# Kernel tuning notes

Hardware: AMD Instinct MI355X
Metric: run time of the kernel (lower is better)

The kernel has to match this reference:

```python
import jax, jax.numpy as jnp
import numpy as np

D_MODEL = 1024
DK = 64
H = D_MODEL // DK
EPS = 1e-5


def setup_inputs() -> dict:
    key = jax.random.key(0)
    ks = jax.random.split(key, 8)
    B, M = 4, 2048
    s = 1.0 / np.sqrt(D_MODEL)
    return {
        "inp": jax.random.normal(ks[0], (B, M, D_MODEL), dtype=jnp.float32),
        "Wq": jax.random.normal(ks[1], (D_MODEL, D_MODEL), dtype=jnp.float32) * s,
        "bq": jnp.zeros((D_MODEL,), dtype=jnp.float32),
        "Wk": jax.random.normal(ks[2], (D_MODEL, D_MODEL), dtype=jnp.float32) * s,
        "bk": jnp.zeros((D_MODEL,), dtype=jnp.float32),
        "Wv": jax.random.normal(ks[3], (D_MODEL, D_MODEL), dtype=jnp.float32) * s,
        "bv": jnp.zeros((D_MODEL,), dtype=jnp.float32),
        "gamma": jnp.ones((D_MODEL,), dtype=jnp.float32),
        "beta": jnp.zeros((D_MODEL,), dtype=jnp.float32),
    }


def reference(inp, Wq, bq, Wk, bk, Wv, bv, gamma, beta):
    B, M, _ = inp.shape
    # LayerNorm over last dim
    mu = jnp.mean(inp, axis=-1, keepdims=True)
    var = jnp.mean(jnp.square(inp - mu), axis=-1, keepdims=True)
    out = (inp - mu) * jax.lax.rsqrt(var + EPS) * gamma + beta
    # QKV projections (x @ W + b)
    Q = (out @ Wq + bq).reshape(B, M, DK, H)
    K = (out @ Wk + bk).reshape(B, M, DK, H)
    V = (out @ Wv + bv).reshape(B, M, DK, H)
    # per-position attention over the dk axis, contracting h
    scores = jnp.einsum("bmih,bmjh->bmij", Q, K) / np.sqrt(DK)  # [B,M,dk,dk]
    att = jax.nn.softmax(scores, axis=-1)
    res = jnp.einsum("bmij,bmjh->bmih", att, V).reshape(B, M, D_MODEL)
    # dropout is identity at eval; positionals add in original is dead code
    return inp + res
```

## Files before the change

kernel.cpp:

```cpp
#include <hip/hip_runtime.h>
#include <hip/hip_bf16.h>

#define D_MODEL 1024
#define NQKV 3072
#define BM 128
#define BN 128
#define BK 32

typedef __attribute__((ext_vector_type(8))) short bf16x8;
typedef __attribute__((ext_vector_type(4))) float f32x4;
typedef __attribute__((ext_vector_type(16))) float f32x16;
typedef __attribute__((ext_vector_type(8))) unsigned short u16x8;

static __device__ __forceinline__ unsigned short f2bf(float f){
  unsigned int x = __float_as_uint(f);
  x += 0x7fff + ((x >> 16) & 1);
  return (unsigned short)(x >> 16);
}
static __device__ __forceinline__ float bf2f(unsigned short u){
  return __uint_as_float(((unsigned int)u) << 16);
}

__global__ __launch_bounds__(256) void ln_kernel(const float* __restrict__ inp,
    const float* __restrict__ gamma, const float* __restrict__ beta,
    unsigned short* __restrict__ X){
  const int row = blockIdx.x;
  const int t = threadIdx.x;
  const float4* ip = (const float4*)(inp + (size_t)row * D_MODEL);
  float4 v = ip[t];
  float s1 = v.x + v.y + v.z + v.w;
  float s2 = v.x*v.x + v.y*v.y + v.z*v.z + v.w*v.w;
#pragma unroll
  for (int off = 32; off >= 1; off >>= 1){
    s1 += __shfl_down(s1, off);
    s2 += __shfl_down(s2, off);
  }
  __shared__ float red[8];
  const int wave = t >> 6, lane = t & 63;
  if (lane == 0){ red[wave] = s1; red[4 + wave] = s2; }
  __syncthreads();
  s1 = red[0] + red[1] + red[2] + red[3];
  s2 = red[4] + red[5] + red[6] + red[7];
  const float mu   = s1 * (1.0f / D_MODEL);
  const float var  = s2 * (1.0f / D_MODEL) - mu * mu;
  const float rstd = rsqrtf(var + 1e-5f);
  float4 g = ((const float4*)gamma)[t];
  float4 b = ((const float4*)beta)[t];
  ushort4 o;
  o.x = f2bf((v.x - mu) * rstd * g.x + b.x);
  o.y = f2bf((v.y - mu) * rstd * g.y + b.y);
  o.z = f2bf((v.z - mu) * rstd * g.z + b.z);
  o.w = f2bf((v.w - mu) * rstd * g.w + b.w);
  ((ushort4*)(X + (size_t)row * D_MODEL))[t] = o;
}

__global__ __launch_bounds__(256) void wtrans_kernel(const float* __restrict__ Wq,
    const float* __restrict__ Wk, const float* __restrict__ Wv,
    unsigned short* __restrict__ Wt){
  __shared__ float tile[32][33];
  const float* W = (blockIdx.z == 0) ? Wq : ((blockIdx.z == 1) ? Wk : Wv);
  const int k0 = blockIdx.x * 32, n0 = blockIdx.y * 32;
  const int r = threadIdx.x >> 5, c = threadIdx.x & 31;
#pragma unroll
  for (int i = 0; i < 4; i++)
    tile[r + i*8][c] = W[(size_t)(k0 + r + i*8) * D_MODEL + n0 + c];
  __syncthreads();
  unsigned short* dst = Wt + (size_t)(blockIdx.z * D_MODEL + n0) * D_MODEL + k0;
#pragma unroll
  for (int i = 0; i < 4; i++){
    int rr = r + i*8;
    dst[(size_t)rr * D_MODEL + c] = f2bf(tile[c][rr]);
  }
}

__global__ void biascat_kernel(const float* __restrict__ bq, const float* __restrict__ bk,
                               const float* __restrict__ bv, float* __restrict__ bc){
  int i = blockIdx.x * 256 + threadIdx.x;
  float v = (i < 1024) ? bq[i] : (i < 2048) ? bk[i - 1024] : bv[i - 2048];
  bc[i] = v;
}

__global__ __launch_bounds__(256) void gemm_kernel(const unsigned short* __restrict__ A,
    const unsigned short* __restrict__ Bt, const float* __restrict__ bias,
    unsigned short* __restrict__ C){
  __shared__ unsigned short As[BM * BK];
  __shared__ unsigned short Bs[BN * BK];
  const int tid = threadIdx.x;
  const int wave = tid >> 6, lane = tid & 63;
  const int wr = wave >> 1, wc = wave & 1;
  const int lr = lane & 15, kg = lane >> 4;
  const int m0 = blockIdx.x * BM, n0 = blockIdx.y * BN;

  f32x4 acc[4][4] = {};

  for (int k0 = 0; k0 < 1024; k0 += BK){
#pragma unroll
    for (int i = 0; i < 2; i++){
      int s = i * 256 + tid;
      int row = s >> 2, cs = s & 3;
      __builtin_amdgcn_global_load_lds(
        (const __attribute__((address_space(1))) void*)(A + (size_t)(m0 + row) * 1024 + k0 + cs * 8),
        (__attribute__((address_space(3))) void*)(As + s * 8), 16, 0, 0);
      __builtin_amdgcn_global_load_lds(
        (const __attribute__((address_space(1))) void*)(Bt + (size_t)(n0 + row) * 1024 + k0 + cs * 8),
        (__attribute__((address_space(3))) void*)(Bs + s * 8), 16, 0, 0);
    }
    __syncthreads();

    bf16x8 a[4], b[4];
    const bf16x8* Ap = (const bf16x8*)As;
    const bf16x8* Bp = (const bf16x8*)Bs;
#pragma unroll
    for (int m = 0; m < 4; m++) a[m] = Ap[(wr*64 + m*16 + lr) * 4 + kg];
#pragma unroll
    for (int n = 0; n < 4; n++) b[n] = Bp[(wc*64 + n*16 + lr) * 4 + kg];
#pragma unroll
    for (int m = 0; m < 4; m++)
#pragma unroll
      for (int n = 0; n < 4; n++)
        acc[m][n] = __builtin_amdgcn_mfma_f32_16x16x32_bf16(a[m], b[n], acc[m][n], 0, 0, 0);
    __syncthreads();
  }

#pragma unroll
  for (int n = 0; n < 4; n++){
    const int gcol = n0 + wc*64 + n*16 + lr;
    const float bb = bias[gcol];
#pragma unroll
    for (int m = 0; m < 4; m++){
      const int gr = m0 + wr*64 + m*16 + kg*4;
#pragma unroll
      for (int r = 0; r < 4; r++)
        C[(size_t)(gr + r) * NQKV + gcol] = f2bf(acc[m][n][r] + bb);
    }
  }
}

__global__ __launch_bounds__(256) void attn_kernel(const unsigned short* __restrict__ qkv,
    const float* __restrict__ inp, float* __restrict__ out){
  __shared__ unsigned short P[4][64 * 64];
  const int wave = threadIdx.x >> 6, lane = threadIdx.x & 63;
  const int token = blockIdx.x * 4 + wave;
  const unsigned short* row = qkv + (size_t)token * NQKV;
  const int l31 = lane & 31, hi = lane >> 5;
  const int l15 = lane & 15, qg = lane >> 4;
  char* pbase = (char*)&P[wave][0];

  bf16x8 kf[2], qf[2];
#pragma unroll
  for (int mt = 0; mt < 2; mt++)
    kf[mt] = *(const bf16x8*)(row + 1024 + (mt*32 + l31)*16 + hi*8);
#pragma unroll
  for (int nt = 0; nt < 2; nt++)
    qf[nt] = *(const bf16x8*)(row + (nt*32 + l31)*16 + hi*8);

  bf16x8 vf[2];
#pragma unroll
  for (int kc = 0; kc < 2; kc++)
#pragma unroll
    for (int e = 0; e < 8; e++)
      vf[kc][e] = (short)row[2048 + (kc*32 + qg*8 + e)*16 + l15];

  f32x16 s[2][2] = {};
#pragma unroll
  for (int mt = 0; mt < 2; mt++)
#pragma unroll
    for (int nt = 0; nt < 2; nt++)
      s[mt][nt] = __builtin_amdgcn_mfma_f32_32x32x16_bf16(kf[mt], qf[nt], s[mt][nt], 0, 0, 0);

#pragma unroll
  for (int ti = 0; ti < 2; ti++){
    float m = s[0][ti][0];
#pragma unroll
    for (int mt = 0; mt < 2; mt++)
#pragma unroll
      for (int r = 0; r < 16; r++) m = fmaxf(m, s[mt][ti][r]);
    m = fmaxf(m, __shfl_xor(m, 32));
    float sum = 0.0f;
#pragma unroll
    for (int mt = 0; mt < 2; mt++)
#pragma unroll
      for (int r = 0; r < 16; r++){
        float p = exp2f((s[mt][ti][r] - m) * 0.1803368801f);
        s[mt][ti][r] = p;
        sum += p;
      }
    sum += __shfl_xor(sum, 32);
    const float invs = 1.0f / sum;
    const int i = ti*32 + l31;
    const int sw = (i & 7) << 4;
#pragma unroll
    for (int mt = 0; mt < 2; mt++)
#pragma unroll
      for (int g = 0; g < 4; g++){
        ushort4 pk;
        pk.x = f2bf(s[mt][ti][4*g + 0] * invs);
        pk.y = f2bf(s[mt][ti][4*g + 1] * invs);
        pk.z = f2bf(s[mt][ti][4*g + 2] * invs);
        pk.w = f2bf(s[mt][ti][4*g + 3] * invs);
        const int jbyte = mt*64 + g*16 + hi*8;
        *(ushort4*)(pbase + ((i*128 + jbyte) ^ sw)) = pk;
      }
  }
  __syncthreads();

  f32x4 o[4] = {};
#pragma unroll
  for (int nt = 0; nt < 4; nt++){
    const int n = nt*16 + l15;
    const int swr = (n & 7) << 4;
#pragma unroll
    for (int kc = 0; kc < 2; kc++){
      bf16x8 pb = *(const bf16x8*)(pbase + ((n*128 + kc*64 + qg*16) ^ swr));
      o[nt] = __builtin_amdgcn_mfma_f32_16x16x32_bf16(vf[kc], pb, o[nt], 0, 0, 0);
    }
  }

  const size_t base = (size_t)token * D_MODEL;
#pragma unroll
  for (int nt = 0; nt < 4; nt++){
    const int i = nt*16 + l15;
    const float4 iv = *(const float4*)(inp + base + i*16 + qg*4);
    float4 ov;
    ov.x = iv.x + o[nt][0];
    ov.y = iv.y + o[nt][1];
    ov.z = iv.z + o[nt][2];
    ov.w = iv.w + o[nt][3];
    *(float4*)(out + base + i*16 + qg*4) = ov;
  }
}

extern "C" void kernel_launch(void* const* d_in, const int* in_sizes, int n_in,
                              void* d_out, int out_size, void* d_ws, size_t ws_size,
                              hipStream_t stream) {
  const float* inp   = (const float*)d_in[0];
  const float* Wq    = (const float*)d_in[1];
  const float* bq    = (const float*)d_in[2];
  const float* Wk    = (const float*)d_in[3];
  const float* bk    = (const float*)d_in[4];
  const float* Wv    = (const float*)d_in[5];
  const float* bv    = (const float*)d_in[6];
  const float* gamma = (const float*)d_in[7];
  const float* beta  = (const float*)d_in[8];
  float* out = (float*)d_out;

  char* ws = (char*)d_ws;
  unsigned short* Xln  = (unsigned short*)ws;
  unsigned short* Wt   = (unsigned short*)(ws + 16777216);
  float*          bc   = (float*)(ws + 23068672);
  unsigned short* QKV  = (unsigned short*)(ws + 23080960);

  ln_kernel<<<8192, 256, 0, stream>>>(inp, gamma, beta, Xln);
  wtrans_kernel<<<dim3(32, 32, 3), 256, 0, stream>>>(Wq, Wk, Wv, Wt);
  biascat_kernel<<<12, 256, 0, stream>>>(bq, bk, bv, bc);
  gemm_kernel<<<dim3(64, 24), 256, 0, stream>>>(Xln, Wt, bc, QKV);
  attn_kernel<<<2048, 256, 0, stream>>>(QKV, inp, out);
}
```

Before: 100.8 us.

## Replace QKV GEMM with 256x256 double-buffered, swizzled-LDS, interleaved-stage kernel

Replaces the 128x128x32 single-buffered GEMM with a 256x256 tile, BK=64, 512-thread kernel. Global-to-LDS loads for the next K tile are issued in four quarter-stages interleaved with MFMA quadrants, using XOR-swizzled LDS addressing to avoid bank conflicts and block-index swizzling for L2 locality. The goal is to hide global load latency behind compute and raise arithmetic intensity. The cost is 128 KB of LDS per block and heavy hand-tuned barriers and waitcnts that rely on exact ordering.

```diff
diff --git a/kernel.cpp b/kernel.cpp
--- a/kernel.cpp
+++ b/kernel.cpp
@@ -3,9 +3,6 @@
 
 #define D_MODEL 1024
 #define NQKV 3072
-#define BM 128
-#define BN 128
-#define BK 32
 
 typedef __attribute__((ext_vector_type(8))) short bf16x8;
 typedef __attribute__((ext_vector_type(4))) float f32x4;
@@ -80,58 +77,127 @@
   bc[i] = v;
 }
 
-__global__ __launch_bounds__(256) void gemm_kernel(const unsigned short* __restrict__ A,
+
+#define STAGE(gbase, xoff, h, tsrc, nb) do { \
+  const char* _s = (gbase) + ((size_t)((h)*128 + r0))*2048 + (size_t)(tsrc)*128 + co; \
+  char* _d = ldsS + (nb)*65536 + (xoff) + (h)*16384 + tid*16; \
+  __builtin_amdgcn_global_load_lds((const __attribute__((address_space(1))) void*)_s, \
+      (__attribute__((address_space(3))) void*)_d, 16, 0, 0); \
+  __builtin_amdgcn_global_load_lds((const __attribute__((address_space(1))) void*)(_s + 131072), \
+      (__attribute__((address_space(3))) void*)(_d + 8192), 16, 0, 0); \
+} while(0)
+
+#define RD_A(qm) do { \
+  _Pragma("unroll") \
+  for (int m2 = 0; m2 < 4; m2++){ \
+    Ar[m2][0] = *(const bf16x8*)(Ab + ((qm)*64 + m2*16)*128 + colb0); \
+    Ar[m2][1] = *(const bf16x8*)(Ab + ((qm)*64 + m2*16)*128 + colb1); \
+  } \
+} while(0)
+
+#define RD_B(qn) do { \
+  _Pragma("unroll") \
+  for (int n2 = 0; n2 < 2; n2++){ \
+    Br[qn][n2][0] = *(const bf16x8*)(Bb + ((qn)*32 + n2*16)*128 + colb0); \
+    Br[qn][n2][1] = *(const bf16x8*)(Bb + ((qn)*32 + n2*16)*128 + colb1); \
+  } \
+} while(0)
+
+#define MFMA_Q(qm, qn) do { \
+  _Pragma("unroll") \
+  for (int m2 = 0; m2 < 4; m2++) \
+    _Pragma("unroll") \
+    for (int n2 = 0; n2 < 2; n2++){ \
+      acc[(qm)*4+m2][(qn)*2+n2] = __builtin_amdgcn_mfma_f32_16x16x32_bf16(Ar[m2][0], Br[qn][n2][0], acc[(qm)*4+m2][(qn)*2+n2], 0, 0, 0); \
+      acc[(qm)*4+m2][(qn)*2+n2] = __builtin_amdgcn_mfma_f32_16x16x32_bf16(Ar[m2][1], Br[qn][n2][1], acc[(qm)*4+m2][(qn)*2+n2], 0, 0, 0); \
+    } \
+} while(0)
+
+#define BARRIER __builtin_amdgcn_s_barrier()
+#define SCHEDB  __builtin_amdgcn_sched_barrier(0)
+#define PRIO1   __builtin_amdgcn_s_setprio(1)
+#define PRIO0   __builtin_amdgcn_s_setprio(0)
+#define VMCNT2  asm volatile("s_waitcnt vmcnt(2)" ::: "memory")
+#define LGKM0   asm volatile("s_waitcnt lgkmcnt(0)" ::: "memory")
+
+__global__ __launch_bounds__(512, 2) void gemm256_kernel(const unsigned short* __restrict__ A,
     const unsigned short* __restrict__ Bt, const float* __restrict__ bias,
     unsigned short* __restrict__ C){
-  __shared__ unsigned short As[BM * BK];
-  __shared__ unsigned short Bs[BN * BK];
+  __shared__ unsigned short ldsAB[2][32768];
+  char* ldsS = (char*)&ldsAB[0][0];
   const int tid = threadIdx.x;
   const int wave = tid >> 6, lane = tid & 63;
-  const int wr = wave >> 1, wc = wave & 1;
-  const int lr = lane & 15, kg = lane >> 4;
-  const int m0 = blockIdx.x * BM, n0 = blockIdx.y * BN;
-
-  f32x4 acc[4][4] = {};
-
-  for (int k0 = 0; k0 < 1024; k0 += BK){
-#pragma unroll
-    for (int i = 0; i < 2; i++){
-      int s = i * 256 + tid;
-      int row = s >> 2, cs = s & 3;
-      __builtin_amdgcn_global_load_lds(
-        (const __attribute__((address_space(1))) void*)(A + (size_t)(m0 + row) * 1024 + k0 + cs * 8),
-        (__attribute__((address_space(3))) void*)(As + s * 8), 16, 0, 0);
-      __builtin_amdgcn_global_load_lds(
-        (const __attribute__((address_space(1))) void*)(Bt + (size_t)(n0 + row) * 1024 + k0 + cs * 8),
-        (__attribute__((address_space(3))) void*)(Bs + s * 8), 16, 0, 0);
-    }
-    __syncthreads();
-
-    bf16x8 a[4], b[4];
-    const bf16x8* Ap = (const bf16x8*)As;
-    const bf16x8* Bp = (const bf16x8*)Bs;
-#pragma unroll
-    for (int m = 0; m < 4; m++) a[m] = Ap[(wr*64 + m*16 + lr) * 4 + kg];
-#pragma unroll
-    for (int n = 0; n < 4; n++) b[n] = Bp[(wc*64 + n*16 + lr) * 4 + kg];
-#pragma unroll
-    for (int m = 0; m < 4; m++)
-#pragma unroll
-      for (int n = 0; n < 4; n++)
-        acc[m][n] = __builtin_amdgcn_mfma_f32_16x16x32_bf16(a[m], b[n], acc[m][n], 0, 0, 0);
-    __syncthreads();
-  }
-
-#pragma unroll
-  for (int n = 0; n < 4; n++){
-    const int gcol = n0 + wc*64 + n*16 + lr;
+  const int wr = wave >> 2, wc = wave & 3;
+  const int lr = lane & 15;
+  const int g16 = (lane >> 4) * 16;
+  const int x7 = (lane & 7) << 4;
+  const int colb0 = g16 ^ x7;
+  const int colb1 = (64 + g16) ^ x7;
+
+  const int b = blockIdx.x;
+  const int swz = (b & 7) * 48 + (b >> 3);
+  const int m0 = (swz & 31) * 256;
+  const int n0 = (swz >> 5) * 256;
+
+  const int r0 = tid >> 3;
+  const size_t co = (size_t)(((tid & 7) * 16) ^ ((r0 & 7) << 4));
+  const char* Ag = (const char*)(A + (size_t)m0 * 1024);
+  const char* Bg = (const char*)(Bt + (size_t)n0 * 1024);
+
+  f32x4 acc[8][4] = {};
+  bf16x8 Ar[4][2], Br[2][2][2];
+
+  STAGE(Ag, 0,     0, 0, 0);
+  STAGE(Bg, 32768, 0, 0, 0);
+  STAGE(Ag, 0,     1, 0, 0);
+  STAGE(Bg, 32768, 1, 0, 0);
+
+  int buf = 0;
+  for (int t = 0; t < 16; ++t, buf ^= 1){
+    const int tn = (t + 1) & 15;
+    const int nb = buf ^ 1;
+    const char* Ab = ldsS + buf*65536 + (wr*128 + lr)*128;
+    const char* Bb = ldsS + buf*65536 + 32768 + (wc*64 + lr)*128;
+
+    STAGE(Ag, 0, 0, tn, nb);
+    VMCNT2;
+    BARRIER;
+    SCHEDB;
+    RD_A(0); RD_B(0);
+    LGKM0; SCHEDB;
+    PRIO1; MFMA_Q(0,0); PRIO0;
+    BARRIER;
+    STAGE(Bg, 32768, 0, tn, nb);
+    RD_B(1);
+    BARRIER;
+    LGKM0; SCHEDB;
+    PRIO1; MFMA_Q(0,1); PRIO0;
+    BARRIER;
+    STAGE(Ag, 0, 1, tn, nb);
+    RD_A(1);
+    BARRIER;
+    LGKM0; SCHEDB;
+    PRIO1; MFMA_Q(1,1); PRIO0;
+    BARRIER;
+    STAGE(Bg, 32768, 1, tn, nb);
+    BARRIER;
+    PRIO1; MFMA_Q(1,0); PRIO0;
+    BARRIER;
+  }
+
+  const int gm = m0 + wr*128;
+  const int gn = n0 + wc*64;
+  const int rr0 = (lane >> 4) * 4;
+#pragma unroll
+  for (int nf = 0; nf < 4; nf++){
+    const int gcol = gn + nf*16 + lr;
     const float bb = bias[gcol];
 #pragma unroll
-    for (int m = 0; m < 4; m++){
-      const int gr = m0 + wr*64 + m*16 + kg*4;
+    for (int mf = 0; mf < 8; mf++){
+      const int grow = gm + mf*16 + rr0;
 #pragma unroll
       for (int r = 0; r < 4; r++)
-        C[(size_t)(gr + r) * NQKV + gcol] = f2bf(acc[m][n][r] + bb);
+        C[(size_t)(grow + r) * NQKV + gcol] = f2bf(acc[mf][nf][r] + bb);
     }
   }
 }
@@ -253,6 +319,6 @@
   ln_kernel<<<8192, 256, 0, stream>>>(inp, gamma, beta, Xln);
   wtrans_kernel<<<dim3(32, 32, 3), 256, 0, stream>>>(Wq, Wk, Wv, Wt);
   biascat_kernel<<<12, 256, 0, stream>>>(bq, bk, bv, bc);
-  gemm_kernel<<<dim3(64, 24), 256, 0, stream>>>(Xln, Wt, bc, QKV);
+  gemm256_kernel<<<384, 512, 0, stream>>>(Xln, Wt, bc, QKV);
   attn_kernel<<<2048, 256, 0, stream>>>(QKV, inp, out);
 }
```

Result: slower. 107.7 us (+6.9%).

## Rewrite QKV GEMM with 128x256 tiles, triple-buffered LDS pipeline and swizzle

Applied to the files above, without the earlier changes.

Replaces the single-buffered 128x128 GEMM with a 512-thread 128x256 tile kernel using BK=64. It prefetches two K tiles ahead into a triple-buffered LDS ring, synchronised with vmcnt waits and raw barriers. It XOR-swizzles the LDS layout to avoid bank conflicts and remaps block IDs for cache locality. The aim is to overlap global loads with MFMA work and cut barrier stalls, at the cost of large LDS use that limits occupancy to one block per CU.

```diff
diff --git a/kernel.cpp b/kernel.cpp
--- a/kernel.cpp
+++ b/kernel.cpp
@@ -3,9 +3,6 @@
 
 #define D_MODEL 1024
 #define NQKV 3072
-#define BM 128
-#define BN 128
-#define BK 32
 
 typedef __attribute__((ext_vector_type(8))) short bf16x8;
 typedef __attribute__((ext_vector_type(4))) float f32x4;
@@ -80,58 +77,96 @@
   bc[i] = v;
 }
 
-__global__ __launch_bounds__(256) void gemm_kernel(const unsigned short* __restrict__ A,
+
+#define GLL(src, dst) __builtin_amdgcn_global_load_lds( \
+    (const __attribute__((address_space(1))) void*)(src), \
+    (__attribute__((address_space(3))) void*)(dst), 16, 0, 0)
+
+#define STAGE(tsrc, bi) do { \
+  const char* _sa = Ag + (size_t)r0*2048 + (size_t)(tsrc)*128 + co; \
+  char* _da = ldsS + (size_t)(bi)*49152 + tid*16; \
+  GLL(_sa, _da); GLL(_sa + 131072, _da + 8192); \
+  const char* _sb = Bg + (size_t)r0*2048 + (size_t)(tsrc)*128 + co; \
+  char* _db = ldsS + (size_t)(bi)*49152 + 16384 + tid*16; \
+  GLL(_sb, _db); GLL(_sb + 131072, _db + 8192); \
+  GLL(_sb + 262144, _db + 16384); GLL(_sb + 393216, _db + 24576); \
+} while(0)
+
+#define BODY(bi) do { \
+  const char* Ab = ldsS + (size_t)(bi)*49152 + (wr*64 + lr)*128; \
+  const char* Bb = ldsS + (size_t)(bi)*49152 + 16384 + (wc*64 + lr)*128; \
+  bf16x8 Ar[4][2], Br[4][2]; \
+  _Pragma("unroll") \
+  for (int m = 0; m < 4; m++){ \
+    Ar[m][0] = *(const bf16x8*)(Ab + m*2048 + colb0); \
+    Ar[m][1] = *(const bf16x8*)(Ab + m*2048 + colb1); \
+  } \
+  _Pragma("unroll") \
+  for (int n = 0; n < 4; n++){ \
+    Br[n][0] = *(const bf16x8*)(Bb + n*2048 + colb0); \
+    Br[n][1] = *(const bf16x8*)(Bb + n*2048 + colb1); \
+  } \
+  _Pragma("unroll") \
+  for (int m = 0; m < 4; m++) \
+    _Pragma("unroll") \
+    for (int n = 0; n < 4; n++){ \
+      acc[m][n] = __builtin_amdgcn_mfma_f32_16x16x32_bf16(Ar[m][0], Br[n][0], acc[m][n], 0, 0, 0); \
+      acc[m][n] = __builtin_amdgcn_mfma_f32_16x16x32_bf16(Ar[m][1], Br[n][1], acc[m][n], 0, 0, 0); \
+    } \
+} while(0)
+
+#define BARRIER __builtin_amdgcn_s_barrier()
+#define SCHEDB  __builtin_amdgcn_sched_barrier(0)
+#define VMCNT6  asm volatile("s_waitcnt vmcnt(6)" ::: "memory")
+#define VMCNT0  asm volatile("s_waitcnt vmcnt(0)" ::: "memory")
+
+__global__ __launch_bounds__(512, 2) void gemm128x256_kernel(const unsigned short* __restrict__ A,
     const unsigned short* __restrict__ Bt, const float* __restrict__ bias,
     unsigned short* __restrict__ C){
-  __shared__ unsigned short As[BM * BK];
-  __shared__ unsigned short Bs[BN * BK];
+  __shared__ __align__(16) char ldsS[3 * 49152];
   const int tid = threadIdx.x;
   const int wave = tid >> 6, lane = tid & 63;
-  const int wr = wave >> 1, wc = wave & 1;
-  const int lr = lane & 15, kg = lane >> 4;
-  const int m0 = blockIdx.x * BM, n0 = blockIdx.y * BN;
+  const int wr = wave >> 2, wc = wave & 3;
+  const int lr = lane & 15;
+  const int colb0 = ((lane >> 4) * 16) ^ ((lane & 7) << 4);
+  const int colb1 = (64 + (lane >> 4) * 16) ^ ((lane & 7) << 4);
+
+  const int b = blockIdx.x;
+  const int swz = (b & 7) * 96 + (b >> 3);
+  const int m0 = (swz & 63) * 128;
+  const int n0 = (swz >> 6) * 256;
+
+  const int r0 = tid >> 3;
+  const size_t co = (size_t)(((tid & 7) * 16) ^ ((r0 & 7) << 4));
+  const char* Ag = (const char*)(A + (size_t)m0 * 1024);
+  const char* Bg = (const char*)(Bt + (size_t)n0 * 1024);
 
   f32x4 acc[4][4] = {};
 
-  for (int k0 = 0; k0 < 1024; k0 += BK){
-#pragma unroll
-    for (int i = 0; i < 2; i++){
-      int s = i * 256 + tid;
-      int row = s >> 2, cs = s & 3;
-      __builtin_amdgcn_global_load_lds(
-        (const __attribute__((address_space(1))) void*)(A + (size_t)(m0 + row) * 1024 + k0 + cs * 8),
-        (__attribute__((address_space(3))) void*)(As + s * 8), 16, 0, 0);
-      __builtin_amdgcn_global_load_lds(
-        (const __attribute__((address_space(1))) void*)(Bt + (size_t)(n0 + row) * 1024 + k0 + cs * 8),
-        (__attribute__((address_space(3))) void*)(Bs + s * 8), 16, 0, 0);
-    }
-    __syncthreads();
-
-    bf16x8 a[4], b[4];
-    const bf16x8* Ap = (const bf16x8*)As;
-    const bf16x8* Bp = (const bf16x8*)Bs;
-#pragma unroll
-    for (int m = 0; m < 4; m++) a[m] = Ap[(wr*64 + m*16 + lr) * 4 + kg];
-#pragma unroll
-    for (int n = 0; n < 4; n++) b[n] = Bp[(wc*64 + n*16 + lr) * 4 + kg];
-#pragma unroll
-    for (int m = 0; m < 4; m++)
-#pragma unroll
-      for (int n = 0; n < 4; n++)
-        acc[m][n] = __builtin_amdgcn_mfma_f32_16x16x32_bf16(a[m], b[n], acc[m][n], 0, 0, 0);
-    __syncthreads();
-  }
-
-#pragma unroll
-  for (int n = 0; n < 4; n++){
-    const int gcol = n0 + wc*64 + n*16 + lr;
+  STAGE(0, 0);
+  STAGE(1, 1);
+
+  for (int t = 0; t < 15; ++t){
+    SCHEDB; VMCNT6; BARRIER; SCHEDB;
+    if (t <= 13) STAGE(t + 2, (t + 2) % 3);
+    BODY(t % 3);
+  }
+  SCHEDB; VMCNT0; BARRIER; SCHEDB;
+  BODY(0);
+
+  const int gm = m0 + wr*64;
+  const int gn = n0 + wc*64;
+  const int rr0 = (lane >> 4) * 4;
+#pragma unroll
+  for (int nf = 0; nf < 4; nf++){
+    const int gcol = gn + nf*16 + lr;
     const float bb = bias[gcol];
 #pragma unroll
-    for (int m = 0; m < 4; m++){
-      const int gr = m0 + wr*64 + m*16 + kg*4;
+    for (int mf = 0; mf < 4; mf++){
+      const int grow = gm + mf*16 + rr0;
 #pragma unroll
       for (int r = 0; r < 4; r++)
-        C[(size_t)(gr + r) * NQKV + gcol] = f2bf(acc[m][n][r] + bb);
+        C[(size_t)(grow + r) * NQKV + gcol] = f2bf(acc[mf][nf][r] + bb);
     }
   }
 }
@@ -253,6 +288,6 @@
   ln_kernel<<<8192, 256, 0, stream>>>(inp, gamma, beta, Xln);
   wtrans_kernel<<<dim3(32, 32, 3), 256, 0, stream>>>(Wq, Wk, Wv, Wt);
   biascat_kernel<<<12, 256, 0, stream>>>(bq, bk, bv, bc);
-  gemm_kernel<<<dim3(64, 24), 256, 0, stream>>>(Xln, Wt, bc, QKV);
+  gemm128x256_kernel<<<768, 512, 0, stream>>>(Xln, Wt, bc, QKV);
   attn_kernel<<<2048, 256, 0, stream>>>(QKV, inp, out);
 }
```

Result: no change. 100.9 us (+0.1%).
